# Performance work log

Hardware: AMD Instinct MI355X
Metric: run time of the kernel (lower is better)

The kernel has to match this reference:

```python
import jax, jax.numpy as jnp
import numpy as np

DIM = 2048
N_HEADS = 16
QK_NOPE = 128
QK_ROPE = 64
V_DIM = 128
QK_DIM = QK_NOPE + QK_ROPE  # 192
B, S = 2, 2048


def setup_inputs() -> dict:
    key = jax.random.key(0)
    ks = jax.random.split(key, 6)
    x = jax.random.normal(ks[0], (B, S, DIM), dtype=jnp.float32)
    # rotary angles: theta[j] = 10000^{-2j/d}, angle[p, j] = p * theta[j]
    inv_freq = 1.0 / (10000.0 ** (np.arange(0, QK_ROPE, 2, dtype=np.float32) / QK_ROPE))
    freqs = jnp.asarray(np.arange(S, dtype=np.float32)[:, None] * inv_freq[None, :])  # [S, QK_ROPE//2]
    # additive causal mask
    mask = jnp.where(jnp.tril(jnp.ones((S, S), dtype=bool)), 0.0, -1e9).astype(jnp.float32)
    sc = 1.0 / np.sqrt(DIM)
    wq = jax.random.normal(ks[1], (DIM, N_HEADS * QK_DIM), dtype=jnp.float32) * sc
    wk = jax.random.normal(ks[2], (DIM, N_HEADS * QK_DIM), dtype=jnp.float32) * sc
    wv = jax.random.normal(ks[3], (DIM, N_HEADS * V_DIM), dtype=jnp.float32) * sc
    wo = jax.random.normal(ks[4], (N_HEADS * V_DIM, DIM), dtype=jnp.float32) * (1.0 / np.sqrt(N_HEADS * V_DIM))
    return {"x": x, "start_pos": 0, "freqs": freqs, "mask": mask,
            "wq": wq, "wk": wk, "wv": wv, "wo": wo}


def _apply_rope(t, freqs):
    # t: [B, S, H, D_rope]; freqs: [S, D_rope//2] angles
    b, s, h, d = t.shape
    tr = t.reshape(b, s, h, d // 2, 2)
    cos = jnp.cos(freqs)[None, :, None, :]
    sin = jnp.sin(freqs)[None, :, None, :]
    out = jnp.stack([tr[..., 0] * cos - tr[..., 1] * sin,
                     tr[..., 0] * sin + tr[..., 1] * cos], axis=-1)
    return out.reshape(b, s, h, d)


def reference(x, start_pos, freqs, mask, wq, wk, wv, wo):
    b, s, _ = x.shape
    xq = x @ wq  # [B,S,H*QK_DIM]
    xk = x @ wk
    xv = (x @ wv).reshape(b, s, N_HEADS, V_DIM)
    qnope, qrope = jnp.split(xq, [N_HEADS * QK_NOPE], axis=-1)
    knope, krope = jnp.split(xk, [N_HEADS * QK_NOPE], axis=-1)
    qnope = qnope.reshape(b, s, N_HEADS, QK_NOPE)
    knope = knope.reshape(b, s, N_HEADS, QK_NOPE)
    qrope = _apply_rope(qrope.reshape(b, s, N_HEADS, QK_ROPE), freqs)
    krope = _apply_rope(krope.reshape(b, s, N_HEADS, QK_ROPE), freqs)
    q = jnp.concatenate([qnope, qrope], axis=-1)  # [B,S,H,QK_DIM]
    k = jnp.concatenate([knope, krope], axis=-1)
    scale = 1.0 / jnp.sqrt(jnp.asarray(QK_DIM, dtype=q.dtype))
    scores = jnp.einsum('bqhd,bkhd->bhqk', q, k) * scale
    scores = scores + mask[None, None, :, :]
    attn = jax.nn.softmax(scores.astype(jnp.float32), axis=-1).astype(scores.dtype)
    out = jnp.einsum('bhqk,bkhd->bqhd', attn, xv)  # [B,S,H,V_DIM]
    out = out.reshape(b, s, N_HEADS * V_DIM)
    return out @ wo
```

## Files before the change

### kernel.cpp

```cpp
#include <hip/hip_runtime.h>
#include <hip/hip_bf16.h>

typedef __attribute__((ext_vector_type(4))) float f32x4;
typedef __attribute__((ext_vector_type(8))) short s16x8;
typedef unsigned int u32;
typedef unsigned short u16;

#define GLDS16(gp, lp) __builtin_amdgcn_global_load_lds(                         \
    (const __attribute__((address_space(1))) u32*)(gp),                          \
    (__attribute__((address_space(3))) u32*)(lp), 16, 0, 0)
#define VMCNT4 asm volatile("s_waitcnt vmcnt(4)" ::: "memory")
#define VMCNT0 asm volatile("s_waitcnt vmcnt(0)" ::: "memory")
#define LGKM8  asm volatile("s_waitcnt lgkmcnt(8)" ::: "memory")
#define LGKM0  asm volatile("s_waitcnt lgkmcnt(0)" ::: "memory")
#define SBAR   __builtin_amdgcn_sched_barrier(0)

__device__ __forceinline__ u16 f2bf(float f) {
    u32 u = __builtin_bit_cast(u32, f);
    u32 r = (u + 0x7FFFu + ((u >> 16) & 1u)) >> 16;
    return (u16)r;
}
__device__ __forceinline__ float bf2f(u16 h) {
    u32 u = ((u32)h) << 16;
    return __builtin_bit_cast(float, u);
}

__global__ __launch_bounds__(256) void conv_f32_bf16(const float4* __restrict__ in,
                                                     ushort4* __restrict__ out, int n4) {
    int i = blockIdx.x * 256 + threadIdx.x;
    if (i < n4) {
        float4 v = in[i];
        ushort4 o;
        o.x = f2bf(v.x); o.y = f2bf(v.y); o.z = f2bf(v.z); o.w = f2bf(v.w);
        out[i] = o;
    }
}

__global__ __launch_bounds__(256) void wtrans(const float* __restrict__ in,
                                              u16* __restrict__ out, int K, int N) {
    __shared__ float tile[32][33];
    int n0 = blockIdx.x * 32, k0 = blockIdx.y * 32;
    int tx = threadIdx.x & 31, ty = threadIdx.x >> 5;
#pragma unroll
    for (int i = 0; i < 4; ++i)
        tile[ty + i * 8][tx] = in[(size_t)(k0 + ty + i * 8) * N + n0 + tx];
    __syncthreads();
#pragma unroll
    for (int i = 0; i < 4; ++i) {
        int n = ty + i * 8;
        out[(size_t)(n0 + n) * K + k0 + tx] = f2bf(tile[tx][n]);
    }
}

__global__ __launch_bounds__(512, 2) void gemm_qkv(const u16* __restrict__ A,
                                                   const u16* __restrict__ W,
                                                   u16* __restrict__ Qh,
                                                   u16* __restrict__ Kh,
                                                   u16* __restrict__ Vn) {
    __shared__ __align__(16) u16 S[2][2][2][128 * 64];
    const int tid = threadIdx.x, lane = tid & 63, wid = tid >> 6;
    const int l15 = lane & 15, l4 = lane >> 4;
    const int id = blockIdx.x;
    const int nt = ((id & 7) << 2) + ((id >> 3) & 3);
    const int mt = id >> 5;
    const int bm0 = mt << 8, bn0 = nt << 8;
    const int wr = wid >> 2, wc = wid & 3;
    f32x4 acc[8][4] = {};

    auto stageH = [&](int mat, int tt, int h) {
        const int kc = tt << 6, p = tt & 1;
        const u16* G = mat ? W : A;
        const int rbase = (mat ? bn0 : bm0) + (h << 7);
        u16* Ld = S[mat][p][h];
#pragma unroll
        for (int j = 0; j < 2; ++j) {
            int c = j * 512 + tid;
            int row = c >> 3, ch = c & 7;
            int cs = ch ^ (row & 7);
            GLDS16(G + (size_t)(rbase + row) * 2048 + kc + cs * 8,
                   (char*)Ld + (j * 512 + wid * 64) * 16);
        }
    };

    s16x8 af[2][2], bfr[4][2];

#define RDA(P, I)                                                              \
    _Pragma("unroll") for (int mm = 0; mm < 2; ++mm)                           \
    _Pragma("unroll") for (int kk = 0; kk < 2; ++kk) {                         \
        int r7 = ((I) * 2 + mm) * 16 + l15;                                    \
        int byt = r7 * 128 + (((kk * 4 + l4) ^ (r7 & 7)) << 4);                \
        af[mm][kk] = *(const s16x8*)((const char*)S[0][P][wr] + byt);          \
    }
#define RDB(P)                                                                 \
    _Pragma("unroll") for (int n = 0; n < 4; ++n)                              \
    _Pragma("unroll") for (int kk = 0; kk < 2; ++kk) {                         \
        int r7 = (wc & 1) * 64 + n * 16 + l15;                                 \
        int byt = r7 * 128 + (((kk * 4 + l4) ^ (r7 & 7)) << 4);                \
        bfr[n][kk] = *(const s16x8*)((const char*)S[1][P][wc >> 1] + byt);     \
    }
#define MF(I)                                                                  \
    __builtin_amdgcn_s_setprio(1);                                             \
    _Pragma("unroll") for (int mm = 0; mm < 2; ++mm)                           \
    _Pragma("unroll") for (int n = 0; n < 4; ++n)                              \
    _Pragma("unroll") for (int kk = 0; kk < 2; ++kk)                           \
        acc[(I) * 2 + mm][n] = __builtin_amdgcn_mfma_f32_16x16x32_bf16(        \
            af[mm][kk], bfr[n][kk], acc[(I) * 2 + mm][n], 0, 0, 0);            \
    __builtin_amdgcn_s_setprio(0);

    stageH(0, 0, 0); stageH(0, 0, 1); stageH(1, 0, 0); stageH(1, 0, 1);
    stageH(0, 1, 0); stageH(0, 1, 1);
    VMCNT4;
    __builtin_amdgcn_s_barrier();
    SBAR;

    for (int t = 0; t < 32; ++t) {
        const int p = t & 1;
        RDB(p); RDA(p, 0);
        if (t == 0) stageH(1, 1, 0);
        else if (t < 31) stageH(0, t + 1, 0);
        LGKM8; SBAR;
        __builtin_amdgcn_s_barrier();
        LGKM0; SBAR;
        MF(0); SBAR;
        __builtin_amdgcn_s_barrier();
        RDA(p, 1);
        if (t == 0) stageH(1, 1, 1);
        else if (t < 31) stageH(0, t + 1, 1);
        __builtin_amdgcn_s_barrier();
        LGKM0; SBAR;
        MF(1); SBAR;
        __builtin_amdgcn_s_barrier();
        RDA(p, 2);
        if (t < 30) stageH(1, t + 2, 0);
        __builtin_amdgcn_s_barrier();
        LGKM0; SBAR;
        MF(2); SBAR;
        __builtin_amdgcn_s_barrier();
        RDA(p, 3);
        if (t < 30) stageH(1, t + 2, 1);
        __builtin_amdgcn_s_barrier();
        LGKM0; SBAR;
        MF(3); SBAR;
        if (t < 31) {
            if (t < 30) { VMCNT4; } else { VMCNT0; }
            SBAR;
        }
        __builtin_amdgcn_s_barrier();
    }
#undef RDA
#undef RDB
#undef MF

#pragma unroll
    for (int m = 0; m < 8; ++m)
#pragma unroll
        for (int n = 0; n < 4; ++n)
#pragma unroll
            for (int r = 0; r < 4; ++r) {
                int row = bm0 + wr * 128 + m * 16 + l4 * 4 + r;
                int c = bn0 + wc * 64 + n * 16 + l15;
                float v = acc[m][n][r];
                if (bn0 >= 6144) {
                    Vn[(size_t)row * 2048 + (c - 6144)] = f2bf(v);
                } else {
                    u16* dst = (bn0 >= 3072) ? Kh : Qh;
                    int cc = (bn0 >= 3072) ? c - 3072 : c;
                    int b = row >> 11, s = row & 2047;
                    int h, d;
                    if (cc < 2048) { h = cc >> 7; d = cc & 127; }
                    else { int mm = cc - 2048; h = mm >> 6; d = 128 + (mm & 63); }
                    dst[(((size_t)b * 16 + h) * 2048 + s) * 192 + d] = f2bf(v);
                }
            }
}

__global__ __launch_bounds__(256) void gemm_bt_f32(const u16* __restrict__ A,
                                                   const u16* __restrict__ Bt,
                                                   float* __restrict__ C,
                                                   int M, int N, int K) {
    __shared__ __align__(16) u16 As[128 * 64];
    __shared__ __align__(16) u16 Bs[128 * 64];
    const int tid = threadIdx.x, lane = tid & 63, wid = tid >> 6;
    const int l15 = lane & 15, l4 = lane >> 4;
    const int bm0 = blockIdx.y << 7, bn0 = blockIdx.x << 7;
    const int wr = wid >> 1, wc = wid & 1;
    f32x4 acc[4][4] = {};
    const int nk = K >> 6;
    for (int t = 0; t < nk; ++t) {
        const int k0 = t << 6;
#pragma unroll
        for (int i = 0; i < 4; ++i) {
            int c = i * 256 + tid;
            int row = c >> 3, c8 = c & 7;
            GLDS16(A + (size_t)(bm0 + row) * K + k0 + c8 * 8,
                   (char*)As + (i * 256 + wid * 64) * 16);
        }
#pragma unroll
        for (int i = 0; i < 4; ++i) {
            int c = i * 256 + tid;
            int row = c >> 3, c8 = c & 7;
            GLDS16(Bt + (size_t)(bn0 + row) * K + k0 + c8 * 8,
                   (char*)Bs + (i * 256 + wid * 64) * 16);
        }
        __syncthreads();
#pragma unroll
        for (int kk = 0; kk < 64; kk += 32) {
            s16x8 af[4], bfr[4];
#pragma unroll
            for (int m = 0; m < 4; ++m)
                af[m] = *(const s16x8*)(As + (wr * 64 + m * 16 + l15) * 64 + kk + l4 * 8);
#pragma unroll
            for (int n = 0; n < 4; ++n)
                bfr[n] = *(const s16x8*)(Bs + (wc * 64 + n * 16 + l15) * 64 + kk + l4 * 8);
#pragma unroll
            for (int m = 0; m < 4; ++m)
#pragma unroll
                for (int n = 0; n < 4; ++n)
                    acc[m][n] = __builtin_amdgcn_mfma_f32_16x16x32_bf16(af[m], bfr[n],
                                                                        acc[m][n], 0, 0, 0);
        }
        __syncthreads();
    }
#pragma unroll
    for (int m = 0; m < 4; ++m)
#pragma unroll
        for (int n = 0; n < 4; ++n)
#pragma unroll
            for (int r = 0; r < 4; ++r) {
                int row = bm0 + wr * 64 + m * 16 + l4 * 4 + r;
                int col = bn0 + wc * 64 + n * 16 + l15;
                C[(size_t)row * N + col] = acc[m][n][r];
            }
}

__global__ __launch_bounds__(256) void rope_inplace(u16* __restrict__ T,
                                                    const float* __restrict__ freqs) {
    int idx = blockIdx.x * 256 + threadIdx.x;
    int j = idx & 31, s = (idx >> 5) & 2047, bh = idx >> 16;
    float ang = freqs[s * 32 + j];
    float c = cosf(ang), sn = sinf(ang);
    u32* p = (u32*)(T + ((size_t)bh * 2048 + s) * 192 + 128) + j;
    u32 v = *p;
    float t0 = bf2f((u16)(v & 0xffff)), t1 = bf2f((u16)(v >> 16));
    float o0 = t0 * c - t1 * sn;
    float o1 = t0 * sn + t1 * c;
    *p = (u32)f2bf(o0) | ((u32)f2bf(o1) << 16);
}

__global__ __launch_bounds__(256) void vtrans(const u16* __restrict__ Vn,
                                              u16* __restrict__ Vt) {
    __shared__ u16 tile[32][33];
    int s0 = blockIdx.x * 32, d0 = blockIdx.y * 32, bh = blockIdx.z;
    int b = bh >> 4, h = bh & 15;
    int tx = threadIdx.x & 31, ty = threadIdx.x >> 5;
#pragma unroll
    for (int i = 0; i < 4; ++i) {
        int s = ty + i * 8;
        tile[s][tx] = Vn[((size_t)b * 2048 + s0 + s) * 2048 + h * 128 + d0 + tx];
    }
    __syncthreads();
#pragma unroll
    for (int i = 0; i < 4; ++i) {
        int d = ty + i * 8;
        Vt[((size_t)bh * 128 + d0 + d) * 2048 + s0 + tx] = tile[tx][d];
    }
}

__global__ __launch_bounds__(256) void attn_fwd3(const u16* __restrict__ Qh,
                                                 const u16* __restrict__ Kh,
                                                 const u16* __restrict__ Vt,
                                                 u16* __restrict__ AO) {
    __shared__ __align__(16) u16 Ks[64 * 192];
    __shared__ __align__(16) u16 Vs[128 * 64];
    __shared__ __align__(16) u16 Ps[4][32 * 64];
    const int tid = threadIdx.x, lane = tid & 63, wid = tid >> 6;
    const int l15 = lane & 15, l4 = lane >> 4;
    const int id = blockIdx.x;
    const int bh = id & 31;
    const int qt = 15 - (id >> 5);
    const int q0 = qt << 7;
    const u16* Qb = Qh + ((size_t)bh * 2048 + q0 + wid * 32) * 192;
    const u16* Kb = Kh + (size_t)bh * 2048 * 192;
    const u16* Vb = Vt + (size_t)bh * 128 * 2048;

    s16x8 aq[2][6];
#pragma unroll
    for (int qg = 0; qg < 2; ++qg)
#pragma unroll
        for (int dk = 0; dk < 6; ++dk)
            aq[qg][dk] = *(const s16x8*)(Qb + (size_t)(qg * 16 + l15) * 192 + dk * 32 + l4 * 8);

    f32x4 acc[2][8] = {};
    float mrow[2][4], lpart[2][4];
#pragma unroll
    for (int qg = 0; qg < 2; ++qg)
#pragma unroll
        for (int r = 0; r < 4; ++r) { mrow[qg][r] = -1e30f; lpart[qg][r] = 0.f; }
    const float scale = 0.07216878364870322f;

    const int ntile = (qt + 1) << 1;
    for (int t = 0; t < ntile; ++t) {
        const int k0 = t << 6;
#pragma unroll
        for (int i = 0; i < 6; ++i) {
            int c = i * 256 + tid;
            int row = (u32)c / 24u, cc = c - row * 24;
            int cs = (cc & 24) | ((cc ^ row) & 7);
            GLDS16(Kb + (size_t)(k0 + row) * 192 + cs * 8,
                   (char*)Ks + (i * 256 + wid * 64) * 16);
        }
#pragma unroll
        for (int i = 0; i < 4; ++i) {
            int c = i * 256 + tid;
            int d = c >> 3, cc = c & 7;
            int cs = cc ^ (d & 7);
            GLDS16(Vb + (size_t)d * 2048 + k0 + cs * 8,
                   (char*)Vs + (i * 256 + wid * 64) * 16);
        }
        __syncthreads();

        if (q0 + wid * 32 + 31 >= k0) {
            f32x4 sc[2][4];
#pragma unroll
            for (int qg = 0; qg < 2; ++qg)
#pragma unroll
                for (int kg = 0; kg < 4; ++kg) sc[qg][kg] = f32x4{0.f, 0.f, 0.f, 0.f};
            __builtin_amdgcn_s_setprio(1);
#pragma unroll
            for (int dk = 0; dk < 6; ++dk) {
                s16x8 bk[4];
#pragma unroll
                for (int kg = 0; kg < 4; ++kg) {
                    int row = kg * 16 + l15;
                    int byt = (row * 384 + dk * 64 + l4 * 16) ^ ((row & 7) << 4);
                    bk[kg] = *(const s16x8*)((const char*)Ks + byt);
                }
#pragma unroll
                for (int qg = 0; qg < 2; ++qg)
#pragma unroll
                    for (int kg = 0; kg < 4; ++kg)
                        sc[qg][kg] = __builtin_amdgcn_mfma_f32_16x16x32_bf16(
                            aq[qg][dk], bk[kg], sc[qg][kg], 0, 0, 0);
            }
            __builtin_amdgcn_s_setprio(0);

            u16* Pw = Ps[wid];
#pragma unroll
            for (int qg = 0; qg < 2; ++qg) {
                const int qrow = q0 + wid * 32 + qg * 16 + l4 * 4;
                const bool domask = (k0 + 63 > qrow);
                float p[4][4], tm[4];
#pragma unroll
                for (int r = 0; r < 4; ++r) tm[r] = -1e30f;
#pragma unroll
                for (int kg = 0; kg < 4; ++kg)
#pragma unroll
                    for (int r = 0; r < 4; ++r) {
                        float v = sc[qg][kg][r] * scale;
                        if (domask && (k0 + kg * 16 + l15 > qrow + r)) v = -1e30f;
                        p[kg][r] = v;
                        tm[r] = fmaxf(tm[r], v);
                    }
#pragma unroll
                for (int off = 1; off < 16; off <<= 1)
#pragma unroll
                    for (int r = 0; r < 4; ++r)
                        tm[r] = fmaxf(tm[r], __shfl_xor(tm[r], off, 64));
                float mn[4];
                bool resc = false;
#pragma unroll
                for (int r = 0; r < 4; ++r) {
                    mn[r] = (tm[r] <= mrow[qg][r] + 8.f) ? mrow[qg][r] : tm[r];
                    resc |= (mn[r] > mrow[qg][r]);
                }
                if (__any(resc)) {
#pragma unroll
                    for (int r = 0; r < 4; ++r) {
                        float scl = __expf(mrow[qg][r] - mn[r]);
                        mrow[qg][r] = mn[r];
                        lpart[qg][r] *= scl;
#pragma unroll
                        for (int db = 0; db < 8; ++db) acc[qg][db][r] *= scl;
                    }
                }
#pragma unroll
                for (int kg = 0; kg < 4; ++kg)
#pragma unroll
                    for (int r = 0; r < 4; ++r) {
                        p[kg][r] = __expf(p[kg][r] - mrow[qg][r]);
                        lpart[qg][r] += p[kg][r];
                    }
#pragma unroll
                for (int kg = 0; kg < 4; ++kg)
#pragma unroll
                    for (int r = 0; r < 4; ++r) {
                        int row = qg * 16 + l4 * 4 + r;
                        int byt = ((row * 64 + kg * 16 + l15) * 2) ^ ((row & 7) << 4);
                        *(u16*)((char*)Pw + byt) = f2bf(p[kg][r]);
                    }
            }

            __builtin_amdgcn_s_setprio(1);
#pragma unroll
            for (int kk = 0; kk < 2; ++kk) {
                s16x8 ap[2];
#pragma unroll
                for (int qg = 0; qg < 2; ++qg) {
                    int row = qg * 16 + l15;
                    int byt = ((row * 64 + kk * 32 + l4 * 8) * 2) ^ ((row & 7) << 4);
                    ap[qg] = *(const s16x8*)((const char*)Pw + byt);
                }
#pragma unroll
                for (int db = 0; db < 8; ++db) {
                    int row = db * 16 + l15;
                    int byt = (row * 128 + kk * 64 + l4 * 16) ^ ((row & 7) << 4);
                    s16x8 bv = *(const s16x8*)((const char*)Vs + byt);
#pragma unroll
                    for (int qg = 0; qg < 2; ++qg)
                        acc[qg][db] = __builtin_amdgcn_mfma_f32_16x16x32_bf16(
                            ap[qg], bv, acc[qg][db], 0, 0, 0);
                }
            }
            __builtin_amdgcn_s_setprio(0);
        }
        __syncthreads();
    }

#pragma unroll
    for (int off = 1; off < 16; off <<= 1)
#pragma unroll
        for (int qg = 0; qg < 2; ++qg)
#pragma unroll
            for (int r = 0; r < 4; ++r)
                lpart[qg][r] += __shfl_xor(lpart[qg][r], off, 64);

    const int b = bh >> 4, h = bh & 15;
#pragma unroll
    for (int qg = 0; qg < 2; ++qg) {
        float inv[4];
#pragma unroll
        for (int r = 0; r < 4; ++r) inv[r] = 1.f / lpart[qg][r];
#pragma unroll
        for (int db = 0; db < 8; ++db)
#pragma unroll
            for (int r = 0; r < 4; ++r) {
                int row = q0 + wid * 32 + qg * 16 + l4 * 4 + r;
                AO[((size_t)b * 2048 + row) * 2048 + h * 128 + db * 16 + l15] =
                    f2bf(acc[qg][db][r] * inv[r]);
            }
    }
}

extern "C" void kernel_launch(void* const* d_in, const int* in_sizes, int n_in,
                              void* d_out, int out_size, void* d_ws, size_t ws_size,
                              hipStream_t stream) {
    const float* x     = (const float*)d_in[0];
    const float* freqs = (const float*)d_in[2];
    const float* wq    = (const float*)d_in[4];
    const float* wk    = (const float*)d_in[5];
    const float* wv    = (const float*)d_in[6];
    const float* wo    = (const float*)d_in[7];
    float* out = (float*)d_out;

    char* ws = (char*)d_ws;
    u16* xb   = (u16*)(ws + 0);
    u16* WT   = (u16*)(ws + 16777216);
    u16* woT  = (u16*)(ws + 50331648);
    u16* Qh   = (u16*)(ws + 58720256);
    u16* Kh   = (u16*)(ws + 83886080);
    u16* Vn   = (u16*)(ws + 109051904);
    u16* Vt   = (u16*)(ws + 125829120);
    u16* AO   = (u16*)(ws + 142606336);

    conv_f32_bf16<<<8192, 256, 0, stream>>>((const float4*)x, (ushort4*)xb, 2097152);
    wtrans<<<dim3(96, 64), 256, 0, stream>>>(wq, WT, 2048, 3072);
    wtrans<<<dim3(96, 64), 256, 0, stream>>>(wk, WT + (size_t)3072 * 2048, 2048, 3072);
    wtrans<<<dim3(64, 64), 256, 0, stream>>>(wv, WT + (size_t)6144 * 2048, 2048, 2048);
    wtrans<<<dim3(64, 64), 256, 0, stream>>>(wo, woT, 2048, 2048);
    gemm_qkv<<<dim3(512), 512, 0, stream>>>(xb, WT, Qh, Kh, Vn);
    rope_inplace<<<8192, 256, 0, stream>>>(Qh, freqs);
    rope_inplace<<<8192, 256, 0, stream>>>(Kh, freqs);
    vtrans<<<dim3(64, 4, 32), 256, 0, stream>>>(Vn, Vt);
    attn_fwd3<<<dim3(512), 256, 0, stream>>>(Qh, Kh, Vt, AO);
    gemm_bt_f32<<<dim3(16, 32), 256, 0, stream>>>(AO, woT, out, 4096, 2048, 2048);
}
```

Before: 359.0 us.

## Fuse RoPE into QKV GEMM epilogue and merge prep kernels into one launch

Applies rotary embedding to Q/K rope columns directly in the QKV GEMM epilogue, exchanging pair elements with a lane shuffle, and removes the separate in-place rope kernels. It also merges the x conversion and four weight-transpose launches into a single prep kernel that dispatches on block index. This is meant to cut launch overhead and an extra read-modify-write pass over Q and K. The cost is transcendental math and freqs loads added to the GEMM epilogue for the rope tiles.

```diff
diff --git a/kernel.cpp b/kernel.cpp
--- a/kernel.cpp
+++ b/kernel.cpp
@@ -25,35 +25,48 @@
     return __builtin_bit_cast(float, u);
 }
 
-__global__ __launch_bounds__(256) void conv_f32_bf16(const float4* __restrict__ in,
-                                                     ushort4* __restrict__ out, int n4) {
-    int i = blockIdx.x * 256 + threadIdx.x;
-    if (i < n4) {
-        float4 v = in[i];
+__global__ __launch_bounds__(256) void prep(const float4* __restrict__ x,
+                                            ushort4* __restrict__ xb4,
+                                            const float* __restrict__ wq,
+                                            const float* __restrict__ wk,
+                                            const float* __restrict__ wv,
+                                            const float* __restrict__ wo,
+                                            u16* __restrict__ WT,
+                                            u16* __restrict__ woT) {
+    __shared__ float tile[32][33];
+    int bid = blockIdx.x;
+    if (bid < 8192) {
+        int i = bid * 256 + threadIdx.x;
+        float4 v = x[i];
         ushort4 o;
         o.x = f2bf(v.x); o.y = f2bf(v.y); o.z = f2bf(v.z); o.w = f2bf(v.w);
-        out[i] = o;
-    }
-}
-
-__global__ __launch_bounds__(256) void wtrans(const float* __restrict__ in,
-                                              u16* __restrict__ out, int K, int N) {
-    __shared__ float tile[32][33];
-    int n0 = blockIdx.x * 32, k0 = blockIdx.y * 32;
+        xb4[i] = o;
+        return;
+    }
+    bid -= 8192;
+    const float* src;
+    u16* dst;
+    int N, bx, by;
+    if (bid < 6144)       { src = wq; dst = WT;                        N = 3072; bx = bid % 96; by = bid / 96; }
+    else if (bid < 12288) { bid -= 6144;  src = wk; dst = WT + (size_t)3072 * 2048; N = 3072; bx = bid % 96; by = bid / 96; }
+    else if (bid < 16384) { bid -= 12288; src = wv; dst = WT + (size_t)6144 * 2048; N = 2048; bx = bid % 64; by = bid / 64; }
+    else                  { bid -= 16384; src = wo; dst = woT;         N = 2048; bx = bid % 64; by = bid / 64; }
+    int n0 = bx * 32, k0 = by * 32;
     int tx = threadIdx.x & 31, ty = threadIdx.x >> 5;
 #pragma unroll
     for (int i = 0; i < 4; ++i)
-        tile[ty + i * 8][tx] = in[(size_t)(k0 + ty + i * 8) * N + n0 + tx];
+        tile[ty + i * 8][tx] = src[(size_t)(k0 + ty + i * 8) * N + n0 + tx];
     __syncthreads();
 #pragma unroll
     for (int i = 0; i < 4; ++i) {
         int n = ty + i * 8;
-        out[(size_t)(n0 + n) * K + k0 + tx] = f2bf(tile[tx][n]);
+        dst[(size_t)(n0 + n) * 2048 + k0 + tx] = f2bf(tile[tx][n]);
     }
 }
 
 __global__ __launch_bounds__(512, 2) void gemm_qkv(const u16* __restrict__ A,
                                                    const u16* __restrict__ W,
+                                                   const float* __restrict__ freqs,
                                                    u16* __restrict__ Qh,
                                                    u16* __restrict__ Kh,
                                                    u16* __restrict__ Vn) {
@@ -151,17 +164,34 @@
 #undef RDB
 #undef MF
 
+    const bool ropeBlk = (bn0 >= 2048 && bn0 < 3072) || (bn0 >= 5120 && bn0 < 6144);
+    const bool evLane = !(l15 & 1);
 #pragma unroll
     for (int m = 0; m < 8; ++m)
 #pragma unroll
-        for (int n = 0; n < 4; ++n)
+        for (int n = 0; n < 4; ++n) {
+            f32x4 v = acc[m][n];
+            if (ropeBlk) {
+                const int j = ((n * 16 + l15) & 63) >> 1;
+#pragma unroll
+                for (int r = 0; r < 4; ++r) {
+                    int row = bm0 + wr * 128 + m * 16 + l4 * 4 + r;
+                    int s = row & 2047;
+                    float ang = freqs[s * 32 + j];
+                    float cs = cosf(ang), sn = sinf(ang);
+                    float other = __shfl_xor(v[r], 1, 64);
+                    float t0 = evLane ? v[r] : other;
+                    float t1 = evLane ? other : v[r];
+                    v[r] = evLane ? (t0 * cs - t1 * sn) : (t0 * sn + t1 * cs);
+                }
+            }
 #pragma unroll
             for (int r = 0; r < 4; ++r) {
                 int row = bm0 + wr * 128 + m * 16 + l4 * 4 + r;
                 int c = bn0 + wc * 64 + n * 16 + l15;
-                float v = acc[m][n][r];
+                float fv = v[r];
                 if (bn0 >= 6144) {
-                    Vn[(size_t)row * 2048 + (c - 6144)] = f2bf(v);
+                    Vn[(size_t)row * 2048 + (c - 6144)] = f2bf(fv);
                 } else {
                     u16* dst = (bn0 >= 3072) ? Kh : Qh;
                     int cc = (bn0 >= 3072) ? c - 3072 : c;
@@ -169,9 +199,10 @@
                     int h, d;
                     if (cc < 2048) { h = cc >> 7; d = cc & 127; }
                     else { int mm = cc - 2048; h = mm >> 6; d = 128 + (mm & 63); }
-                    dst[(((size_t)b * 16 + h) * 2048 + s) * 192 + d] = f2bf(v);
-                }
-            }
+                    dst[(((size_t)b * 16 + h) * 2048 + s) * 192 + d] = f2bf(fv);
+                }
+            }
+        }
 }
 
 __global__ __launch_bounds__(256) void gemm_bt_f32(const u16* __restrict__ A,
@@ -231,20 +262,6 @@
                 int col = bn0 + wc * 64 + n * 16 + l15;
                 C[(size_t)row * N + col] = acc[m][n][r];
             }
-}
-
-__global__ __launch_bounds__(256) void rope_inplace(u16* __restrict__ T,
-                                                    const float* __restrict__ freqs) {
-    int idx = blockIdx.x * 256 + threadIdx.x;
-    int j = idx & 31, s = (idx >> 5) & 2047, bh = idx >> 16;
-    float ang = freqs[s * 32 + j];
-    float c = cosf(ang), sn = sinf(ang);
-    u32* p = (u32*)(T + ((size_t)bh * 2048 + s) * 192 + 128) + j;
-    u32 v = *p;
-    float t0 = bf2f((u16)(v & 0xffff)), t1 = bf2f((u16)(v >> 16));
-    float o0 = t0 * c - t1 * sn;
-    float o1 = t0 * sn + t1 * c;
-    *p = (u32)f2bf(o0) | ((u32)f2bf(o1) << 16);
 }
 
 __global__ __launch_bounds__(256) void vtrans(const u16* __restrict__ Vn,
@@ -472,14 +489,9 @@
     u16* Vt   = (u16*)(ws + 125829120);
     u16* AO   = (u16*)(ws + 142606336);
 
-    conv_f32_bf16<<<8192, 256, 0, stream>>>((const float4*)x, (ushort4*)xb, 2097152);
-    wtrans<<<dim3(96, 64), 256, 0, stream>>>(wq, WT, 2048, 3072);
-    wtrans<<<dim3(96, 64), 256, 0, stream>>>(wk, WT + (size_t)3072 * 2048, 2048, 3072);
-    wtrans<<<dim3(64, 64), 256, 0, stream>>>(wv, WT + (size_t)6144 * 2048, 2048, 2048);
-    wtrans<<<dim3(64, 64), 256, 0, stream>>>(wo, woT, 2048, 2048);
-    gemm_qkv<<<dim3(512), 512, 0, stream>>>(xb, WT, Qh, Kh, Vn);
-    rope_inplace<<<8192, 256, 0, stream>>>(Qh, freqs);
-    rope_inplace<<<8192, 256, 0, stream>>>(Kh, freqs);
+    prep<<<28672, 256, 0, stream>>>((const float4*)x, (ushort4*)xb,
+                                    wq, wk, wv, wo, WT, woT);
+    gemm_qkv<<<dim3(512), 512, 0, stream>>>(xb, WT, freqs, Qh, Kh, Vn);
     vtrans<<<dim3(64, 4, 32), 256, 0, stream>>>(Vn, Vt);
     attn_fwd3<<<dim3(512), 256, 0, stream>>>(Qh, Kh, Vt, AO);
     gemm_bt_f32<<<dim3(16, 32), 256, 0, stream>>>(AO, woT, out, 4096, 2048, 2048);
```

Result: slower. 484.0 us (+34.8%).
